# Kernel tuning notes

Hardware: AMD Instinct MI355X
Metric: run time of the kernel (lower is better)

The kernel has to match this reference:

```python
import jax, jax.numpy as jnp
import numpy as np

NUM_HEADS = 16
HEAD_DIM = 128
QUERY_DIM = 2048
SCALE = HEAD_DIM ** -0.5


def setup_inputs() -> dict:
    key = jax.random.key(0)
    ks = jax.random.split(key, 11)
    B, L, D = 2, 2048, QUERY_DIM
    HD = NUM_HEADS * HEAD_DIM
    s = 0.02
    return {
        "x_q": jax.random.normal(ks[0], (B, L, D), jnp.float32),
        "x_k": jax.random.normal(ks[1], (B, L, D), jnp.float32),
        "x_v": jax.random.normal(ks[2], (B, L, D), jnp.float32),
        "Wq": jax.random.normal(ks[3], (D, HD), jnp.float32) * s,
        "bq": jnp.zeros((HD,), jnp.float32),
        "Wk": jax.random.normal(ks[4], (D, HD), jnp.float32) * s,
        "bk": jnp.zeros((HD,), jnp.float32),
        "Wv": jax.random.normal(ks[5], (D, HD), jnp.float32) * s,
        "bv": jnp.zeros((HD,), jnp.float32),
        "Wo": jax.random.normal(ks[6], (HD, D), jnp.float32) * s,
        "bo": jnp.zeros((D,), jnp.float32),
    }


def _split_heads(x):  # [b, l, h*d] -> [b, h, l, d]
    b, l, _ = x.shape
    return x.reshape(b, l, NUM_HEADS, HEAD_DIM).transpose(0, 2, 1, 3)


def reference(x_q, x_k, x_v, Wq, bq, Wk, bk, Wv, bv, Wo, bo):
    # Note: the torch module constructs norm_q/norm_k but NEVER applies them in forward.
    q = _split_heads(x_q @ Wq + bq)  # [b, h, l, d]
    k = _split_heads(x_k @ Wk + bk)
    v = _split_heads(x_v @ Wv + bv)
    scores = jnp.einsum("bhid,bhjd->bhij", q, k) * SCALE
    probs = jax.nn.softmax(scores, axis=-1)
    o = jnp.einsum("bhij,bhjd->bhid", probs, v)  # [b, h, l, d]
    b, h, l, d = o.shape
    o = o.transpose(0, 2, 1, 3).reshape(b, l, h * d)
    return o @ Wo + bo
```

## Files before the change

### kernel.cpp

```cpp
#include <hip/hip_runtime.h>


typedef _Float16 f16;
typedef __attribute__((ext_vector_type(8))) _Float16 f16x8;
typedef __attribute__((ext_vector_type(4))) _Float16 f16x4;
typedef __attribute__((ext_vector_type(4))) float f32x4;
typedef __attribute__((ext_vector_type(4))) unsigned int u32x4;

#define QSCALE (0.08838834764831845f * 1.4426950408889634f)
#define SWZ3(r) (((r) & 3) | (((r) >> 1) & 4))
#define SWZV(r) ((r) & 7)

static __device__ __forceinline__ void gload16(void* lds, const void* g) {
  __builtin_amdgcn_global_load_lds(
      (__attribute__((address_space(1))) void*)g,
      (__attribute__((address_space(3))) void*)lds, 16, 0, 0);
}

__global__ __launch_bounds__(256) void cvt_x_kernel(
    const float* __restrict__ x0, const float* __restrict__ x1,
    const float* __restrict__ x2, f16* __restrict__ out) {
  const float* x = blockIdx.z == 0 ? x0 : (blockIdx.z == 1 ? x1 : x2);
  f16* o = out + (size_t)blockIdx.z * 8388608;
  size_t i = ((size_t)blockIdx.x * 256 + threadIdx.x) * 8;
  f32x4 a = *(const f32x4*)(x + i);
  f32x4 b = *(const f32x4*)(x + i + 4);
  f16x8 r;
  r[0] = (f16)a[0]; r[1] = (f16)a[1]; r[2] = (f16)a[2]; r[3] = (f16)a[3];
  r[4] = (f16)b[0]; r[5] = (f16)b[1]; r[6] = (f16)b[2]; r[7] = (f16)b[3];
  *(f16x8*)(o + i) = r;
}

__global__ __launch_bounds__(256) void cvt_w_kernel(
    const float* __restrict__ w0, const float* __restrict__ w1,
    const float* __restrict__ w2, const float* __restrict__ w3,
    f16* __restrict__ out) {
  const float* W = blockIdx.z == 0 ? w0 : blockIdx.z == 1 ? w1
                 : blockIdx.z == 2 ? w2 : w3;
  f16* WT = out + (size_t)blockIdx.z * 4194304;
  __shared__ f16 tile[64][68];
  const int tx = threadIdx.x & 15, ty = threadIdx.x >> 4;
  const int k0 = blockIdx.y * 64, n0 = blockIdx.x * 64;
#pragma unroll
  for (int i = 0; i < 4; ++i) {
    int r = ty + i * 16;
    f32x4 v = *(const f32x4*)(W + (size_t)(k0 + r) * 2048 + n0 + tx * 4);
    tile[r][tx * 4 + 0] = (f16)v[0]; tile[r][tx * 4 + 1] = (f16)v[1];
    tile[r][tx * 4 + 2] = (f16)v[2]; tile[r][tx * 4 + 3] = (f16)v[3];
  }
  __syncthreads();
#pragma unroll
  for (int i = 0; i < 4; ++i) {
    int n = ty + i * 16;
    f16x4 o;
    o[0] = tile[tx * 4 + 0][n]; o[1] = tile[tx * 4 + 1][n];
    o[2] = tile[tx * 4 + 2][n]; o[3] = tile[tx * 4 + 3][n];
    *(f16x4*)(WT + (size_t)(n0 + n) * 2048 + k0 + tx * 4) = o;
  }
}

template <int MODE>
__global__ __launch_bounds__(512, 2) void gemm128_kernel(
    const f16* __restrict__ Abase, const f16* __restrict__ Btbase,
    void* __restrict__ Obase, const float* __restrict__ b0,
    const float* __restrict__ b1, const float* __restrict__ b2) {
  const int lid = blockIdx.x;
  int bn, bm, z;
  if (MODE == 0) {
    const int logi = (lid & 7) * 96 + (lid >> 3);
    bn = logi & 7; bm = (logi >> 3) & 31; z = logi >> 8;
  } else {
    const int logi = (lid & 7) * 32 + (lid >> 3);
    bn = logi & 7; bm = logi >> 3; z = 0;
  }
  const f16* A  = Abase  + (size_t)z * 8388608;
  const f16* Bt = Btbase + (size_t)z * 4194304;
  const float* bias = z == 0 ? b0 : (z == 1 ? b1 : b2);
  const float qsc = (MODE == 0 && z == 0) ? QSCALE : 1.0f;
  const int tid = threadIdx.x, lane = tid & 63, w = tid >> 6;
  const int wm = w >> 2, wn = w & 3;
  const int l15 = lane & 15, lg = lane >> 4;
  __shared__ alignas(16) char smb[98304];

  f32x4 acc[4][4];
#pragma unroll
  for (int i = 0; i < 4; ++i)
#pragma unroll
    for (int j = 0; j < 4; ++j) acc[i][j] = (f32x4)0.f;

#define GSTAGE(KT, C_)                                                        \
  {                                                                           \
    char* Ab_ = smb + (C_) * 49152;                                           \
    char* Bb_ = Ab_ + 16384;                                                  \
    _Pragma("unroll") for (int p = 0; p < 2; ++p) {                           \
      int L = p * 8192 + tid * 16;                                            \
      int row = L >> 7, pcol = L & 127;                                       \
      int scol = pcol ^ ((row & 7) << 4);                                     \
      gload16(Ab_ + L,                                                        \
              (const char*)A + ((size_t)(bm * 128 + row) * 2048 + (KT) * 64) * 2 + scol); \
    }                                                                         \
    _Pragma("unroll") for (int p = 0; p < 4; ++p) {                           \
      int L = p * 8192 + tid * 16;                                            \
      int row = L >> 7, pcol = L & 127;                                       \
      int scol = pcol ^ ((row & 7) << 4);                                     \
      gload16(Bb_ + L,                                                        \
              (const char*)Bt + ((size_t)(bn * 256 + row) * 2048 + (KT) * 64) * 2 + scol); \
    }                                                                         \
  }

#define GREADS(H)                                                             \
  _Pragma("unroll") for (int i = 0; i < 4; ++i) {                             \
    int row = wm * 64 + i * 16 + l15;                                         \
    af[H][i] = *(const f16x8*)(Ab + row * 128 +                               \
                               (((H) * 64 + lg * 16) ^ ((row & 7) << 4)));    \
  }                                                                           \
  _Pragma("unroll") for (int j = 0; j < 4; ++j) {                             \
    int row = wn * 64 + j * 16 + l15;                                         \
    bf[H][j] = *(const f16x8*)(Bb + row * 128 +                               \
                               (((H) * 64 + lg * 16) ^ ((row & 7) << 4)));    \
  }

#define GMFMA(H)                                                              \
  __builtin_amdgcn_s_setprio(1);                                              \
  _Pragma("unroll") for (int i = 0; i < 4; ++i)                               \
    _Pragma("unroll") for (int j = 0; j < 4; ++j)                             \
      acc[i][j] = __builtin_amdgcn_mfma_f32_16x16x32_f16(                     \
          af[H][i], bf[H][j], acc[i][j], 0, 0, 0);                            \
  __builtin_amdgcn_s_setprio(0);

  GSTAGE(0, 0);
#pragma unroll 1
  for (int kt = 0; kt < 32; ++kt) {
    const int c = kt & 1;
    if (kt < 31) {
      GSTAGE(kt + 1, c ^ 1);
      asm volatile("s_waitcnt vmcnt(6)" ::: "memory");
    } else {
      asm volatile("s_waitcnt vmcnt(0)" ::: "memory");
    }
    __builtin_amdgcn_s_barrier();

    const char* Ab = smb + c * 49152;
    const char* Bb = Ab + 16384;
    f16x8 af[2][4], bf[2][4];
    GREADS(0);
    asm volatile("s_waitcnt lgkmcnt(0)" ::: "memory");
    __builtin_amdgcn_sched_barrier(0);
    GMFMA(0);
    GREADS(1);
    __builtin_amdgcn_sched_barrier(0);
    __builtin_amdgcn_s_barrier();
    asm volatile("s_waitcnt lgkmcnt(0)" ::: "memory");
    __builtin_amdgcn_sched_barrier(0);
    GMFMA(1);
  }

  if (MODE == 0 && z == 2) {
    char* lt = smb;
    __syncthreads();
#pragma unroll
    for (int i = 0; i < 4; ++i)
#pragma unroll
      for (int j = 0; j < 4; ++j) {
        int dl = wn * 64 + j * 16 + l15;
        float bv = bias[bn * 256 + dl];
        f16x4 vv;
#pragma unroll
        for (int r = 0; r < 4; ++r) vv[r] = (f16)(acc[i][j][r] + bv);
        *(f16x4*)(lt + dl * 272 + (wm * 64 + i * 16 + lg * 4) * 2) = vv;
      }
    __syncthreads();
    f16* Vt = (f16*)Obase + (size_t)2 * 8388608;
    const int b_ = bm >> 4;
    const int lb = (bm & 15) * 128;
#pragma unroll
    for (int cpar = 0; cpar < 8; ++cpar) {
      int cid = cpar * 512 + tid;
      int dl = cid >> 4, o8 = cid & 15;
      f16x8 vv = *(const f16x8*)(lt + dl * 272 + o8 * 16);
      int dg = bn * 256 + dl, h = dg >> 7, dh = dg & 127;
      *(f16x8*)(Vt + (size_t)(b_ * 16 + h) * 262144 + (size_t)dh * 2048 +
                lb + o8 * 8) = vv;
    }
  } else if (MODE == 0) {
    f16* Oz = (f16*)Obase + (size_t)z * 8388608;
#pragma unroll
    for (int i = 0; i < 4; ++i)
#pragma unroll
      for (int j = 0; j < 4; ++j) {
        int col = bn * 256 + wn * 64 + j * 16 + l15;
        int h = col >> 7, d = col & 127;
        float bv = bias[col];
#pragma unroll
        for (int r = 0; r < 4; ++r) {
          int rowg = bm * 128 + wm * 64 + i * 16 + lg * 4 + r;
          int b_ = rowg >> 11, lpos = rowg & 2047;
          Oz[(size_t)(b_ * 16 + h) * 262144 + (size_t)lpos * 128 + d] =
              (f16)((acc[i][j][r] + bv) * qsc);
        }
      }
  } else {
    float* Out = (float*)Obase;
#pragma unroll
    for (int i = 0; i < 4; ++i)
#pragma unroll
      for (int j = 0; j < 4; ++j) {
        int col = bn * 256 + wn * 64 + j * 16 + l15;
        float bv = bias[col];
#pragma unroll
        for (int r = 0; r < 4; ++r) {
          int rowg = bm * 128 + wm * 64 + i * 16 + lg * 4 + r;
          Out[(size_t)rowg * 2048 + col] = acc[i][j][r] + bv;
        }
      }
  }
#undef GSTAGE
#undef GREADS
#undef GMFMA
}

__global__ __launch_bounds__(512, 4) void attn_kernel(
    const f16* __restrict__ q, const f16* __restrict__ k,
    const f16* __restrict__ vt, f16* __restrict__ o) {
  const int orig = blockIdx.y * 16 + blockIdx.x;
  const int swz = (orig & 7) * 64 + (orig >> 3);
  const int qt = swz & 15, bh = swz >> 4;
  const int tid = threadIdx.x, lane = tid & 63, w = tid >> 6;
  const int l15 = lane & 15, lg = lane >> 4;
  const f16* Qb = q + (size_t)bh * 262144 + (size_t)qt * 128 * 128;
  const char* Kb = (const char*)(k + (size_t)bh * 262144);
  const char* Vtb = (const char*)(vt + (size_t)bh * 262144);
  __shared__ alignas(16) char sm[65536];

  f16x8 qf[4];
#pragma unroll
  for (int ks = 0; ks < 4; ++ks)
    qf[ks] = *(const f16x8*)(Qb + (w * 16 + l15) * 128 + ks * 32 + lg * 8);

  f32x4 oacc[8];
#pragma unroll
  for (int df = 0; df < 8; ++df) oacc[df] = (f32x4)0.f;
  float mrow = -1e30f, ps = 0.f;
  const int rA = ((l15 >> 2) << 3) + (l15 & 3);

#define STAGE(T, B)                                                          \
  {                                                                          \
    char* Ks_ = sm + (B) * 32768;                                            \
    char* Vs_ = Ks_ + 16384;                                                 \
    _Pragma("unroll") for (int i = 0; i < 2; ++i) {                          \
      int c = i * 8 + w;                                                     \
      int phys = c * 1024 + lane * 16;                                       \
      {                                                                      \
        int row = phys >> 8, pcol = phys & 255;                              \
        int lcol = pcol ^ (SWZ3(row) << 4);                                  \
        gload16(Ks_ + c * 1024, Kb + (size_t)((T) * 64 + row) * 256 + lcol); \
      }                                                                      \
      {                                                                      \
        int row = phys >> 7, pcol = phys & 127;                              \
        int lcol = pcol ^ (SWZV(row) << 4);                                  \
        gload16(Vs_ + c * 1024, Vtb + (size_t)row * 4096 + (T) * 128 + lcol);\
      }                                                                      \
    }                                                                        \
  }

  STAGE(0, 0);
  int cur = 0;
  for (int t = 0; t < 32; ++t) {
    __syncthreads();
    if (t < 31) STAGE(t + 1, cur ^ 1);
    const char* Ks = sm + cur * 32768;
    const char* Vs = Ks + 16384;

    f32x4 s[4];
#pragma unroll
    for (int nf = 0; nf < 4; ++nf) s[nf] = (f32x4)0.f;
    __builtin_amdgcn_s_setprio(1);
#pragma unroll
    for (int ks = 0; ks < 4; ++ks) {
      f16x8 kf[4];
#pragma unroll
      for (int nf = 0; nf < 4; ++nf) {
        int row = ((nf & 1) << 5) + ((nf >> 1) << 2) + rA;
        int colb = (ks * 64 + lg * 16) ^ (SWZ3(row) << 4);
        kf[nf] = *(const f16x8*)(Ks + row * 256 + colb);
      }
#pragma unroll
      for (int nf = 0; nf < 4; ++nf)
        s[nf] = __builtin_amdgcn_mfma_f32_16x16x32_f16(kf[nf], qf[ks], s[nf], 0, 0, 0);
    }
    __builtin_amdgcn_s_setprio(0);

    unsigned int pk[2][4];
    {
      float m0 = fmaxf(fmaxf(s[0][0], s[0][1]), fmaxf(s[0][2], s[0][3]));
      float m1 = fmaxf(fmaxf(s[1][0], s[1][1]), fmaxf(s[1][2], s[1][3]));
      float m2 = fmaxf(fmaxf(s[2][0], s[2][1]), fmaxf(s[2][2], s[2][3]));
      float m3 = fmaxf(fmaxf(s[3][0], s[3][1]), fmaxf(s[3][2], s[3][3]));
      float mx = fmaxf(fmaxf(m0, m1), fmaxf(m2, m3));
      mx = fmaxf(mx, __shfl_xor(mx, 16));
      mx = fmaxf(mx, __shfl_xor(mx, 32));
      if (!__all(mx <= mrow + 8.f)) {
        float mnew = fmaxf(mrow, mx);
        float sc = exp2f(mrow - mnew);
        mrow = mnew;
        ps *= sc;
#pragma unroll
        for (int r = 0; r < 4; ++r) {
          float scr = __shfl(sc, (lane & 48) | (lg * 4 + r));
#pragma unroll
          for (int df = 0; df < 8; ++df) oacc[df][r] *= scr;
        }
      }
      float m = mrow;
      float psum = 0.f;
#pragma unroll
      for (int nf = 0; nf < 4; ++nf)
#pragma unroll
        for (int h = 0; h < 2; ++h) {
          float p0 = exp2f(s[nf][2 * h] - m);
          float p1 = exp2f(s[nf][2 * h + 1] - m);
          psum += p0 + p1;
          pk[nf & 1][(nf >> 1) * 2 + h] =
              __builtin_bit_cast(unsigned int, __builtin_amdgcn_cvt_pkrtz(p0, p1));
        }
      ps += psum;
    }

    __builtin_amdgcn_s_setprio(1);
#pragma unroll
    for (int kvs = 0; kvs < 2; ++kvs) {
      f16x8 pa = __builtin_bit_cast(f16x8, *(const u32x4*)pk[kvs]);
#pragma unroll
      for (int df = 0; df < 8; ++df) {
        int row = df * 16 + l15;
        int colb = (kvs * 64 + lg * 16) ^ (SWZV(row) << 4);
        f16x8 vb = *(const f16x8*)(Vs + row * 128 + colb);
        oacc[df] = __builtin_amdgcn_mfma_f32_16x16x32_f16(pa, vb, oacc[df], 0, 0, 0);
      }
    }
    __builtin_amdgcn_s_setprio(0);
    cur ^= 1;
  }

  const int b_ = bh >> 4, h_ = bh & 15;
  f16* Ob = o + (size_t)b_ * 4194304 + (size_t)qt * 128 * 2048 + h_ * 128;
  float lr = ps;
  lr += __shfl_xor(lr, 16);
  lr += __shfl_xor(lr, 32);
  float inv = 1.f / lr;
#pragma unroll
  for (int r = 0; r < 4; ++r) {
    float invr = __shfl(inv, (lane & 48) | (lg * 4 + r));
    int rl = w * 16 + lg * 4 + r;
#pragma unroll
    for (int df = 0; df < 8; ++df)
      Ob[(size_t)rl * 2048 + df * 16 + l15] = (f16)(oacc[df][r] * invr);
  }
#undef STAGE
}

extern "C" void kernel_launch(void* const* d_in, const int* in_sizes, int n_in,
                              void* d_out, int out_size, void* d_ws, size_t ws_size,
                              hipStream_t stream) {
  const float* xq = (const float*)d_in[0];
  const float* xk = (const float*)d_in[1];
  const float* xv = (const float*)d_in[2];
  const float* Wq = (const float*)d_in[3];
  const float* bq = (const float*)d_in[4];
  const float* Wk = (const float*)d_in[5];
  const float* bk = (const float*)d_in[6];
  const float* Wv = (const float*)d_in[7];
  const float* bv = (const float*)d_in[8];
  const float* Wo = (const float*)d_in[9];
  const float* bo = (const float*)d_in[10];

  char* ws = (char*)d_ws;
  f16* xh   = (f16*)(ws);
  f16* wt   = (f16*)(ws + 50331648);
  f16* qkv  = (f16*)(ws + 83886080);
  f16* oatt = (f16*)(ws + 16777216);
  float* outp = (float*)d_out;

  hipLaunchKernelGGL(cvt_x_kernel, dim3(4096, 1, 3), dim3(256), 0, stream,
                     xq, xk, xv, xh);
  hipLaunchKernelGGL(cvt_w_kernel, dim3(32, 32, 4), dim3(256), 0, stream,
                     Wq, Wk, Wv, Wo, wt);
  hipLaunchKernelGGL((gemm128_kernel<0>), dim3(768), dim3(512), 0, stream,
                     xh, wt, (void*)qkv, bq, bk, bv);
  hipLaunchKernelGGL(attn_kernel, dim3(16, 32), dim3(512), 0, stream,
                     qkv, qkv + (size_t)8388608, qkv + (size_t)2 * 8388608, oatt);
  hipLaunchKernelGGL((gemm128_kernel<1>), dim3(256), dim3(512), 0, stream,
                     oatt, wt + (size_t)3 * 4194304, (void*)outp, bo, bo, bo);
}
```

Before: 287.2 us.

## Fuse fp32-to-fp16 activation conversion into QKV projection GEMM A-load

Removes the separate cvt_x kernel and has the QKV GEMM read fp32 activations directly into registers, convert them to fp16, and store them swizzled into LDS. The loads for the next tile are issued early and written after the first MFMA half, keeping double buffering. This avoids writing and re-reading a 48MB fp16 copy of the inputs and one kernel launch. In exchange the GEMM reads twice the A bytes and does register-staged stores instead of direct global-to-LDS loads, which adds VGPR pressure and VALU work in the main loop.

```diff
diff --git a/kernel.cpp b/kernel.cpp
--- a/kernel.cpp
+++ b/kernel.cpp
@@ -15,20 +15,6 @@
   __builtin_amdgcn_global_load_lds(
       (__attribute__((address_space(1))) void*)g,
       (__attribute__((address_space(3))) void*)lds, 16, 0, 0);
-}
-
-__global__ __launch_bounds__(256) void cvt_x_kernel(
-    const float* __restrict__ x0, const float* __restrict__ x1,
-    const float* __restrict__ x2, f16* __restrict__ out) {
-  const float* x = blockIdx.z == 0 ? x0 : (blockIdx.z == 1 ? x1 : x2);
-  f16* o = out + (size_t)blockIdx.z * 8388608;
-  size_t i = ((size_t)blockIdx.x * 256 + threadIdx.x) * 8;
-  f32x4 a = *(const f32x4*)(x + i);
-  f32x4 b = *(const f32x4*)(x + i + 4);
-  f16x8 r;
-  r[0] = (f16)a[0]; r[1] = (f16)a[1]; r[2] = (f16)a[2]; r[3] = (f16)a[3];
-  r[4] = (f16)b[0]; r[5] = (f16)b[1]; r[6] = (f16)b[2]; r[7] = (f16)b[3];
-  *(f16x8*)(o + i) = r;
 }
 
 __global__ __launch_bounds__(256) void cvt_w_kernel(
@@ -61,7 +47,8 @@
 
 template <int MODE>
 __global__ __launch_bounds__(512, 2) void gemm128_kernel(
-    const f16* __restrict__ Abase, const f16* __restrict__ Btbase,
+    const void* __restrict__ A0, const void* __restrict__ A1,
+    const void* __restrict__ A2, const f16* __restrict__ Btbase,
     void* __restrict__ Obase, const float* __restrict__ b0,
     const float* __restrict__ b1, const float* __restrict__ b2) {
   const int lid = blockIdx.x;
@@ -73,7 +60,8 @@
     const int logi = (lid & 7) * 32 + (lid >> 3);
     bn = logi & 7; bm = logi >> 3; z = 0;
   }
-  const f16* A  = Abase  + (size_t)z * 8388608;
+  const float* Af = (const float*)(z == 0 ? A0 : (z == 1 ? A1 : A2));
+  const f16* Ah = (const f16*)A0;
   const f16* Bt = Btbase + (size_t)z * 4194304;
   const float* bias = z == 0 ? b0 : (z == 1 ? b1 : b2);
   const float qsc = (MODE == 0 && z == 0) ? QSCALE : 1.0f;
@@ -88,23 +76,51 @@
 #pragma unroll
     for (int j = 0; j < 4; ++j) acc[i][j] = (f32x4)0.f;
 
-#define GSTAGE(KT, C_)                                                        \
+  const int arow = tid >> 2, akoff = (tid & 3) * 16;
+  f32x4 a0, a1, a2, a3;
+
+#define GLOADA(KT)                                                            \
+  {                                                                           \
+    const float* src = Af + (size_t)(bm * 128 + arow) * 2048 + (KT) * 64 + akoff; \
+    a0 = *(const f32x4*)(src);      a1 = *(const f32x4*)(src + 4);            \
+    a2 = *(const f32x4*)(src + 8);  a3 = *(const f32x4*)(src + 12);           \
+  }
+
+#define GSTOREA(C_)                                                           \
   {                                                                           \
     char* Ab_ = smb + (C_) * 49152;                                           \
-    char* Bb_ = Ab_ + 16384;                                                  \
-    _Pragma("unroll") for (int p = 0; p < 2; ++p) {                           \
-      int L = p * 8192 + tid * 16;                                            \
-      int row = L >> 7, pcol = L & 127;                                       \
-      int scol = pcol ^ ((row & 7) << 4);                                     \
-      gload16(Ab_ + L,                                                        \
-              (const char*)A + ((size_t)(bm * 128 + row) * 2048 + (KT) * 64) * 2 + scol); \
+    int o = (tid & 3) * 32;                                                   \
+    int swz = (arow & 7) << 4;                                                \
+    f16x8 w0_, w1_;                                                           \
+    _Pragma("unroll") for (int r = 0; r < 4; ++r) {                           \
+      w0_[r] = (f16)a0[r]; w0_[4 + r] = (f16)a1[r];                           \
+      w1_[r] = (f16)a2[r]; w1_[4 + r] = (f16)a3[r];                           \
     }                                                                         \
+    *(f16x8*)(Ab_ + arow * 128 + (o ^ swz)) = w0_;                            \
+    *(f16x8*)(Ab_ + arow * 128 + ((o + 16) ^ swz)) = w1_;                     \
+  }
+
+#define BSTAGE(KT, C_)                                                        \
+  {                                                                           \
+    char* Bb_ = smb + (C_) * 49152 + 16384;                                   \
     _Pragma("unroll") for (int p = 0; p < 4; ++p) {                           \
       int L = p * 8192 + tid * 16;                                            \
       int row = L >> 7, pcol = L & 127;                                       \
       int scol = pcol ^ ((row & 7) << 4);                                     \
       gload16(Bb_ + L,                                                        \
               (const char*)Bt + ((size_t)(bn * 256 + row) * 2048 + (KT) * 64) * 2 + scol); \
+    }                                                                         \
+  }
+
+#define ASTAGE16(KT, C_)                                                      \
+  {                                                                           \
+    char* Ab_ = smb + (C_) * 49152;                                           \
+    _Pragma("unroll") for (int p = 0; p < 2; ++p) {                           \
+      int L = p * 8192 + tid * 16;                                            \
+      int row = L >> 7, pcol = L & 127;                                       \
+      int scol = pcol ^ ((row & 7) << 4);                                     \
+      gload16(Ab_ + L,                                                        \
+              (const char*)Ah + ((size_t)(bm * 128 + row) * 2048 + (KT) * 64) * 2 + scol); \
     }                                                                         \
   }
 
@@ -128,13 +144,31 @@
           af[H][i], bf[H][j], acc[i][j], 0, 0, 0);                            \
   __builtin_amdgcn_s_setprio(0);
 
-  GSTAGE(0, 0);
+  if (MODE == 0) {
+    GLOADA(0);
+    BSTAGE(0, 0);
+    GSTOREA(0);
+    asm volatile("s_waitcnt lgkmcnt(0)" ::: "memory");
+  } else {
+    ASTAGE16(0, 0);
+    BSTAGE(0, 0);
+  }
+
 #pragma unroll 1
   for (int kt = 0; kt < 32; ++kt) {
     const int c = kt & 1;
     if (kt < 31) {
-      GSTAGE(kt + 1, c ^ 1);
-      asm volatile("s_waitcnt vmcnt(6)" ::: "memory");
+      if (MODE == 0) {
+        GLOADA(kt + 1);
+        BSTAGE(kt + 1, c ^ 1);
+        __builtin_amdgcn_sched_barrier(0);
+        asm volatile("s_waitcnt vmcnt(8)" ::: "memory");
+      } else {
+        ASTAGE16(kt + 1, c ^ 1);
+        BSTAGE(kt + 1, c ^ 1);
+        __builtin_amdgcn_sched_barrier(0);
+        asm volatile("s_waitcnt vmcnt(6)" ::: "memory");
+      }
     } else {
       asm volatile("s_waitcnt vmcnt(0)" ::: "memory");
     }
@@ -147,6 +181,7 @@
     asm volatile("s_waitcnt lgkmcnt(0)" ::: "memory");
     __builtin_amdgcn_sched_barrier(0);
     GMFMA(0);
+    if (MODE == 0 && kt < 31) GSTOREA(c ^ 1);
     GREADS(1);
     __builtin_amdgcn_sched_barrier(0);
     __builtin_amdgcn_s_barrier();
@@ -214,7 +249,10 @@
         }
       }
   }
-#undef GSTAGE
+#undef GLOADA
+#undef GSTOREA
+#undef BSTAGE
+#undef ASTAGE16
 #undef GREADS
 #undef GMFMA
 }
@@ -375,20 +413,19 @@
   const float* bo = (const float*)d_in[10];
 
   char* ws = (char*)d_ws;
-  f16* xh   = (f16*)(ws);
+  f16* oatt = (f16*)(ws);
   f16* wt   = (f16*)(ws + 50331648);
   f16* qkv  = (f16*)(ws + 83886080);
-  f16* oatt = (f16*)(ws + 16777216);
   float* outp = (float*)d_out;
 
-  hipLaunchKernelGGL(cvt_x_kernel, dim3(4096, 1, 3), dim3(256), 0, stream,
-                     xq, xk, xv, xh);
   hipLaunchKernelGGL(cvt_w_kernel, dim3(32, 32, 4), dim3(256), 0, stream,
                      Wq, Wk, Wv, Wo, wt);
   hipLaunchKernelGGL((gemm128_kernel<0>), dim3(768), dim3(512), 0, stream,
-                     xh, wt, (void*)qkv, bq, bk, bv);
+                     (const void*)xq, (const void*)xk, (const void*)xv, wt,
+                     (void*)qkv, bq, bk, bv);
   hipLaunchKernelGGL(attn_kernel, dim3(16, 32), dim3(512), 0, stream,
                      qkv, qkv + (size_t)8388608, qkv + (size_t)2 * 8388608, oatt);
   hipLaunchKernelGGL((gemm128_kernel<1>), dim3(256), dim3(512), 0, stream,
-                     oatt, wt + (size_t)3 * 4194304, (void*)outp, bo, bo, bo);
+                     (const void*)oatt, nullptr, nullptr,
+                     wt + (size_t)3 * 4194304, (void*)outp, bo, bo, bo);
 }
```

New measurement: 323.0 us. +12.5%, slower.

## Double attention query tile per block and triple-buffer K/V staging

Applied to the files above, without the earlier changes.

Each attention block now handles 256 query rows, two 16-row fragments per wave, instead of 128. Every K/V tile loaded into shared memory is therefore reused across twice as many queries, halving K/V global traffic and LDS staging per query. The K/V pipeline moves from double to triple buffering with explicit vmcnt waits, so loads run two tiles ahead. In exchange the grid shrinks to 256 blocks, register pressure roughly doubles (launch bounds drop to 2 blocks per CU), and LDS use grows to 96KB.

```diff
diff --git a/kernel.cpp b/kernel.cpp
--- a/kernel.cpp
+++ b/kernel.cpp
@@ -219,28 +219,34 @@
 #undef GMFMA
 }
 
-__global__ __launch_bounds__(512, 4) void attn_kernel(
+__global__ __launch_bounds__(512, 2) void attn_kernel(
     const f16* __restrict__ q, const f16* __restrict__ k,
     const f16* __restrict__ vt, f16* __restrict__ o) {
-  const int orig = blockIdx.y * 16 + blockIdx.x;
-  const int swz = (orig & 7) * 64 + (orig >> 3);
-  const int qt = swz & 15, bh = swz >> 4;
+  const int orig = blockIdx.x;
+  const int swz = (orig & 7) * 32 + (orig >> 3);
+  const int qt = swz & 7, bh = swz >> 3;
   const int tid = threadIdx.x, lane = tid & 63, w = tid >> 6;
   const int l15 = lane & 15, lg = lane >> 4;
-  const f16* Qb = q + (size_t)bh * 262144 + (size_t)qt * 128 * 128;
+  const f16* Qb = q + (size_t)bh * 262144 + (size_t)qt * 256 * 128;
   const char* Kb = (const char*)(k + (size_t)bh * 262144);
   const char* Vtb = (const char*)(vt + (size_t)bh * 262144);
-  __shared__ alignas(16) char sm[65536];
-
-  f16x8 qf[4];
-#pragma unroll
-  for (int ks = 0; ks < 4; ++ks)
-    qf[ks] = *(const f16x8*)(Qb + (w * 16 + l15) * 128 + ks * 32 + lg * 8);
-
-  f32x4 oacc[8];
-#pragma unroll
-  for (int df = 0; df < 8; ++df) oacc[df] = (f32x4)0.f;
-  float mrow = -1e30f, ps = 0.f;
+  __shared__ alignas(16) char sm[98304];
+
+  f16x8 qf[2][4];
+#pragma unroll
+  for (int mf = 0; mf < 2; ++mf)
+#pragma unroll
+    for (int ks = 0; ks < 4; ++ks)
+      qf[mf][ks] = *(const f16x8*)(Qb + (w * 32 + mf * 16 + l15) * 128 + ks * 32 + lg * 8);
+
+  f32x4 oacc[2][8];
+  float mrow[2], ps[2];
+#pragma unroll
+  for (int mf = 0; mf < 2; ++mf) {
+#pragma unroll
+    for (int df = 0; df < 8; ++df) oacc[mf][df] = (f32x4)0.f;
+    mrow[mf] = -1e30f; ps[mf] = 0.f;
+  }
   const int rA = ((l15 >> 2) << 3) + (l15 & 3);
 
 #define STAGE(T, B)                                                          \
@@ -264,16 +270,24 @@
   }
 
   STAGE(0, 0);
+  STAGE(1, 1);
   int cur = 0;
+  int nxt2 = 2;
   for (int t = 0; t < 32; ++t) {
-    __syncthreads();
-    if (t < 31) STAGE(t + 1, cur ^ 1);
+    if (t < 31)
+      asm volatile("s_waitcnt vmcnt(4)" ::: "memory");
+    else
+      asm volatile("s_waitcnt vmcnt(0)" ::: "memory");
+    __builtin_amdgcn_s_barrier();
+    if (t < 30) STAGE(t + 2, nxt2);
     const char* Ks = sm + cur * 32768;
     const char* Vs = Ks + 16384;
 
-    f32x4 s[4];
-#pragma unroll
-    for (int nf = 0; nf < 4; ++nf) s[nf] = (f32x4)0.f;
+    f32x4 s[2][4];
+#pragma unroll
+    for (int mf = 0; mf < 2; ++mf)
+#pragma unroll
+      for (int nf = 0; nf < 4; ++nf) s[mf][nf] = (f32x4)0.f;
     __builtin_amdgcn_s_setprio(1);
 #pragma unroll
     for (int ks = 0; ks < 4; ++ks) {
@@ -285,76 +299,92 @@
         kf[nf] = *(const f16x8*)(Ks + row * 256 + colb);
       }
 #pragma unroll
-      for (int nf = 0; nf < 4; ++nf)
-        s[nf] = __builtin_amdgcn_mfma_f32_16x16x32_f16(kf[nf], qf[ks], s[nf], 0, 0, 0);
+      for (int mf = 0; mf < 2; ++mf)
+#pragma unroll
+        for (int nf = 0; nf < 4; ++nf)
+          s[mf][nf] = __builtin_amdgcn_mfma_f32_16x16x32_f16(kf[nf], qf[mf][ks], s[mf][nf], 0, 0, 0);
     }
     __builtin_amdgcn_s_setprio(0);
 
-    unsigned int pk[2][4];
-    {
-      float m0 = fmaxf(fmaxf(s[0][0], s[0][1]), fmaxf(s[0][2], s[0][3]));
-      float m1 = fmaxf(fmaxf(s[1][0], s[1][1]), fmaxf(s[1][2], s[1][3]));
-      float m2 = fmaxf(fmaxf(s[2][0], s[2][1]), fmaxf(s[2][2], s[2][3]));
-      float m3 = fmaxf(fmaxf(s[3][0], s[3][1]), fmaxf(s[3][2], s[3][3]));
-      float mx = fmaxf(fmaxf(m0, m1), fmaxf(m2, m3));
+    unsigned int pk[2][2][4];
+#pragma unroll
+    for (int mf = 0; mf < 2; ++mf) {
+      float m01 = fmaxf(fmaxf(s[mf][0][0], s[mf][0][1]),
+                        fmaxf(s[mf][0][2], s[mf][0][3]));
+      float m23 = fmaxf(fmaxf(s[mf][1][0], s[mf][1][1]),
+                        fmaxf(s[mf][1][2], s[mf][1][3]));
+      float m45 = fmaxf(fmaxf(s[mf][2][0], s[mf][2][1]),
+                        fmaxf(s[mf][2][2], s[mf][2][3]));
+      float m67 = fmaxf(fmaxf(s[mf][3][0], s[mf][3][1]),
+                        fmaxf(s[mf][3][2], s[mf][3][3]));
+      float mx = fmaxf(fmaxf(m01, m23), fmaxf(m45, m67));
       mx = fmaxf(mx, __shfl_xor(mx, 16));
       mx = fmaxf(mx, __shfl_xor(mx, 32));
-      if (!__all(mx <= mrow + 8.f)) {
-        float mnew = fmaxf(mrow, mx);
-        float sc = exp2f(mrow - mnew);
-        mrow = mnew;
-        ps *= sc;
+      if (!__all(mx <= mrow[mf] + 8.f)) {
+        float mnew = fmaxf(mrow[mf], mx);
+        float sc = exp2f(mrow[mf] - mnew);
+        mrow[mf] = mnew;
+        ps[mf] *= sc;
 #pragma unroll
         for (int r = 0; r < 4; ++r) {
           float scr = __shfl(sc, (lane & 48) | (lg * 4 + r));
 #pragma unroll
-          for (int df = 0; df < 8; ++df) oacc[df][r] *= scr;
+          for (int df = 0; df < 8; ++df) oacc[mf][df][r] *= scr;
         }
       }
-      float m = mrow;
+      float m = mrow[mf];
       float psum = 0.f;
 #pragma unroll
       for (int nf = 0; nf < 4; ++nf)
 #pragma unroll
         for (int h = 0; h < 2; ++h) {
-          float p0 = exp2f(s[nf][2 * h] - m);
-          float p1 = exp2f(s[nf][2 * h + 1] - m);
+          float p0 = exp2f(s[mf][nf][2 * h] - m);
+          float p1 = exp2f(s[mf][nf][2 * h + 1] - m);
           psum += p0 + p1;
-          pk[nf & 1][(nf >> 1) * 2 + h] =
+          pk[mf][nf & 1][(nf >> 1) * 2 + h] =
               __builtin_bit_cast(unsigned int, __builtin_amdgcn_cvt_pkrtz(p0, p1));
         }
-      ps += psum;
+      ps[mf] += psum;
     }
 
     __builtin_amdgcn_s_setprio(1);
 #pragma unroll
     for (int kvs = 0; kvs < 2; ++kvs) {
-      f16x8 pa = __builtin_bit_cast(f16x8, *(const u32x4*)pk[kvs]);
+      f16x8 pa[2];
+#pragma unroll
+      for (int mf = 0; mf < 2; ++mf)
+        pa[mf] = __builtin_bit_cast(f16x8, *(const u32x4*)pk[mf][kvs]);
 #pragma unroll
       for (int df = 0; df < 8; ++df) {
         int row = df * 16 + l15;
         int colb = (kvs * 64 + lg * 16) ^ (SWZV(row) << 4);
         f16x8 vb = *(const f16x8*)(Vs + row * 128 + colb);
-        oacc[df] = __builtin_amdgcn_mfma_f32_16x16x32_f16(pa, vb, oacc[df], 0, 0, 0);
+#pragma unroll
+        for (int mf = 0; mf < 2; ++mf)
+          oacc[mf][df] = __builtin_amdgcn_mfma_f32_16x16x32_f16(pa[mf], vb, oacc[mf][df], 0, 0, 0);
       }
     }
     __builtin_amdgcn_s_setprio(0);
-    cur ^= 1;
+    cur = cur == 2 ? 0 : cur + 1;
+    nxt2 = nxt2 == 2 ? 0 : nxt2 + 1;
   }
 
   const int b_ = bh >> 4, h_ = bh & 15;
-  f16* Ob = o + (size_t)b_ * 4194304 + (size_t)qt * 128 * 2048 + h_ * 128;
-  float lr = ps;
-  lr += __shfl_xor(lr, 16);
-  lr += __shfl_xor(lr, 32);
-  float inv = 1.f / lr;
-#pragma unroll
-  for (int r = 0; r < 4; ++r) {
-    float invr = __shfl(inv, (lane & 48) | (lg * 4 + r));
-    int rl = w * 16 + lg * 4 + r;
-#pragma unroll
-    for (int df = 0; df < 8; ++df)
-      Ob[(size_t)rl * 2048 + df * 16 + l15] = (f16)(oacc[df][r] * invr);
+  f16* Ob = o + (size_t)b_ * 4194304 + (size_t)qt * 256 * 2048 + h_ * 128;
+#pragma unroll
+  for (int mf = 0; mf < 2; ++mf) {
+    float lr = ps[mf];
+    lr += __shfl_xor(lr, 16);
+    lr += __shfl_xor(lr, 32);
+    float inv = 1.f / lr;
+#pragma unroll
+    for (int r = 0; r < 4; ++r) {
+      float invr = __shfl(inv, (lane & 48) | (lg * 4 + r));
+      int rl = w * 32 + mf * 16 + lg * 4 + r;
+#pragma unroll
+      for (int df = 0; df < 8; ++df)
+        Ob[(size_t)rl * 2048 + df * 16 + l15] = (f16)(oacc[mf][df][r] * invr);
+    }
   }
 #undef STAGE
 }
@@ -387,7 +417,7 @@
                      Wq, Wk, Wv, Wo, wt);
   hipLaunchKernelGGL((gemm128_kernel<0>), dim3(768), dim3(512), 0, stream,
                      xh, wt, (void*)qkv, bq, bk, bv);
-  hipLaunchKernelGGL(attn_kernel, dim3(16, 32), dim3(512), 0, stream,
+  hipLaunchKernelGGL(attn_kernel, dim3(256), dim3(512), 0, stream,
                      qkv, qkv + (size_t)8388608, qkv + (size_t)2 * 8388608, oatt);
   hipLaunchKernelGGL((gemm128_kernel<1>), dim3(256), dim3(512), 0, stream,
                      oatt, wt + (size_t)3 * 4194304, (void*)outp, bo, bo, bo);
```

After: 286.2 us, median of 2. Within noise of the previous version (-0.3%).
